# Kernel tuning notes

Measured on AMD Instinct MI355X. Metric: run time of the kernel, lower is better.

## Reference

```python
import jax, jax.numpy as jnp
import numpy as np

B = 2_097_152          # batch of theta samples
POLY_DEG = 127         # QSP polynomial degree -> 128 phases
PI = np.float32(np.pi)


def setup_inputs() -> dict:
    key = jax.random.key(0)
    k1, k2 = jax.random.split(key)
    th = jax.random.uniform(k1, (B, 1), dtype=jnp.float32) * PI
    phis = jax.random.uniform(k2, (POLY_DEG + 1, 1), dtype=jnp.float32) * PI
    return {"th": th, "phis": phis}


def reference(th, phis):
    # th: [B,1] float32, phis: [P+1,1] float32 (learned QSP phases)
    theta = th[:, 0]                      # [B]
    c = jnp.cos(theta)
    s = jnp.sin(theta)
    # expm(i*theta*X) = cos(theta) I + i sin(theta) X  (closed form, no expm)
    wx = jnp.stack(
        [jnp.stack([c + 0j, 1j * s], axis=-1),
         jnp.stack([1j * s, c + 0j], axis=-1)],
        axis=-2,
    ).astype(jnp.complex64)               # [B,2,2]

    phi = phis[:, 0]                      # [P+1]
    e = jnp.exp(1j * phi).astype(jnp.complex64)
    # expm(i*phi*Z) = diag(e^{i phi}, e^{-i phi})
    rz = (jnp.zeros((phi.shape[0], 2, 2), jnp.complex64)
          .at[:, 0, 0].set(e)
          .at[:, 1, 1].set(jnp.conj(e)))  # [P+1,2,2]

    u0 = jnp.broadcast_to(rz[0], (theta.shape[0], 2, 2))  # [B,2,2]

    def step(u, rzk):
        u = jnp.einsum('bij,bjk->bik', u, wx)   # u @ W(x)
        u = jnp.einsum('bij,jk->bik', u, rzk)   # ... @ Rz(phi_k)
        return u, None

    u, _ = jax.lax.scan(step, u0, rz[1:])       # 127 sequential steps
    # convention == 0: (Re[u_00], Im[u_00])
    return (jnp.real(u[:, 0, 0]), jnp.imag(u[:, 0, 0]))
```

## Files before the change

kernel.cpp:

```cpp
#include <hip/hip_runtime.h>


typedef float v2f __attribute__((ext_vector_type(2)));

#define NPHI 128

__global__ __launch_bounds__(256, 8) void qsp_fused(
    const float* __restrict__ th,
    const float* __restrict__ phis,
    float* __restrict__ out,
    int Bq)
{
    __shared__ float2 g2[NPHI];
    __shared__ float2 e[NPHI];

    const int tid = threadIdx.x;

    if (tid < 64) {
        const int L = tid;
        float sp, cp;
        __sincosf(phis[L], &sp, &cp);
        e[L] = make_float2(cp, sp);
        __sincosf(phis[L + 64], &sp, &cp);
        e[L + 64] = make_float2(cp, sp);

        float Ar0 = 0.f, Ai0 = 0.f, Br0 = 0.f, Bi0 = 0.f;
        float Ar1 = 0.f, Ai1 = 0.f, Br1 = 0.f, Bi1 = 0.f;
        const float2 e0 = e[0];
        if (L == 0) { Ar0 = e0.x; Ai0 = e0.y; }

        for (int k = 1; k < NPHI; ++k) {
            const float2 ek = e[k];
            float pAr = __shfl_up(Ar1, 1, 64);
            float pAi = __shfl_up(Ai1, 1, 64);
            float pBr = __shfl_up(Br1, 1, 64);
            float pBi = __shfl_up(Bi1, 1, 64);
            if (L == 0) { pAr = 0.f; pAi = 0.f; pBr = 0.f; pBi = 0.f; }
            const float s0Ar = 0.5f * (pAr + Ar0 + pBr - Br0);
            const float s0Ai = 0.5f * (pAi + Ai0 + pBi - Bi0);
            const float s0Br = 0.5f * (pAr - Ar0 + pBr + Br0);
            const float s0Bi = 0.5f * (pAi - Ai0 + pBi + Bi0);
            const float s1Ar = 0.5f * (Ar0 + Ar1 + Br0 - Br1);
            const float s1Ai = 0.5f * (Ai0 + Ai1 + Bi0 - Bi1);
            const float s1Br = 0.5f * (Ar0 - Ar1 + Br0 + Br1);
            const float s1Bi = 0.5f * (Ai0 - Ai1 + Bi0 + Bi1);
            Ar0 = ek.x * s0Ar - ek.y * s0Ai;  Ai0 = ek.x * s0Ai + ek.y * s0Ar;
            Br0 = ek.x * s0Br + ek.y * s0Bi;  Bi0 = ek.x * s0Bi - ek.y * s0Br;
            Ar1 = ek.x * s1Ar - ek.y * s1Ai;  Ai1 = ek.x * s1Ai + ek.y * s1Ar;
            Br1 = ek.x * s1Br + ek.y * s1Bi;  Bi1 = ek.x * s1Bi - ek.y * s1Br;
        }
        g2[2 * L]     = make_float2(Ar0, Ai0);
        g2[2 * L + 1] = make_float2(Ar1, Ai1);
    }

    const int idx = blockIdx.x * blockDim.x + tid;
    const int lidx = (idx < Bq) ? idx : 0;
    const float4 t4 = ((const float4*)th)[lidx];

    float zs0, zc0, zs1, zc1, zs2, zc2, zs3, zc3;
    __sincosf(2.f * t4.x, &zs0, &zc0);
    __sincosf(2.f * t4.y, &zs1, &zc1);
    __sincosf(2.f * t4.z, &zs2, &zc2);
    __sincosf(2.f * t4.w, &zs3, &zc3);
    const v2f zrA = {zc0, zc1}, ziA = {zs0, zs1}, nziA = {-zs0, -zs1};
    const v2f zrB = {zc2, zc3}, ziB = {zs2, zs3}, nziB = {-zs2, -zs3};

    float S0, C0, S1, C1, S2, C2, S3, C3;
    __sincosf(127.f * t4.x, &S0, &C0);
    __sincosf(127.f * t4.y, &S1, &C1);
    __sincosf(127.f * t4.z, &S2, &C2);
    __sincosf(127.f * t4.w, &S3, &C3);

    __syncthreads();

    const float2 gt = g2[NPHI - 1];
    v2f arA = {gt.x, gt.x}, aiA = {gt.y, gt.y};
    v2f arB = arA,          aiB = aiA;

    #pragma unroll 4
    for (int j = NPHI - 2; j >= 0; --j) {
        const float2 gj = g2[j];
        const v2f gr = {gj.x, gj.x};
        const v2f gi = {gj.y, gj.y};
        const v2f nrA = __builtin_elementwise_fma(
            arA, zrA, __builtin_elementwise_fma(aiA, nziA, gr));
        const v2f niA = __builtin_elementwise_fma(
            arA, ziA, __builtin_elementwise_fma(aiA, zrA, gi));
        const v2f nrB = __builtin_elementwise_fma(
            arB, zrB, __builtin_elementwise_fma(aiB, nziB, gr));
        const v2f niB = __builtin_elementwise_fma(
            arB, ziB, __builtin_elementwise_fma(aiB, zrB, gi));
        arA = nrA; aiA = niA;
        arB = nrB; aiB = niB;
    }

    const v2f CA = {C0, C1}, SA = {S0, S1};
    const v2f CB = {C2, C3}, SB = {S2, S3};
    const v2f orA = __builtin_elementwise_fma(arA, CA, aiA * SA);
    const v2f oiA = __builtin_elementwise_fma(aiA, CA, -(arA * SA));
    const v2f orB = __builtin_elementwise_fma(arB, CB, aiB * SB);
    const v2f oiB = __builtin_elementwise_fma(aiB, CB, -(arB * SB));

    if (idx < Bq) {
        ((float4*)out)[idx]      = make_float4(orA.x, orA.y, orB.x, orB.y);
        ((float4*)out)[idx + Bq] = make_float4(oiA.x, oiA.y, oiB.x, oiB.y);
    }
}

extern "C" void kernel_launch(void* const* d_in, const int* in_sizes, int n_in,
                              void* d_out, int out_size, void* d_ws, size_t ws_size,
                              hipStream_t stream)
{
    const float* th   = (const float*)d_in[0];
    const float* phis = (const float*)d_in[1];
    float* out = (float*)d_out;
    const int B = in_sizes[0];
    const int Bq = B >> 2;
    const int block = 256;
    const int grid = (Bq + block - 1) / block;
    qsp_fused<<<grid, block, 0, stream>>>(th, phis, out, Bq);
}
```

Before: 103.2 us.

## Use 1024-thread blocks and pack-vectorize the per-block phase-coefficient recurrence

Block size grows from 256 to 1024, so the redundant per-block 127-step wavefront that turns phases into polynomial coefficients runs once for every 1024 samples instead of every 256. That recurrence is also rewritten on packed two-float vectors, with the 0.5 factor folded into the precomputed phase exponentials, to cut its instruction count. The costs are a 1024-wide __syncthreads where 960 threads wait on one wavefront, and launch bounds of (1024, 8) that may constrain registers.

```diff
diff --git a/kernel.cpp b/kernel.cpp
--- a/kernel.cpp
+++ b/kernel.cpp
@@ -5,14 +5,14 @@
 
 #define NPHI 128
 
-__global__ __launch_bounds__(256, 8) void qsp_fused(
+__global__ __launch_bounds__(1024, 8) void qsp_fused(
     const float* __restrict__ th,
     const float* __restrict__ phis,
     float* __restrict__ out,
     int Bq)
 {
     __shared__ float2 g2[NPHI];
-    __shared__ float2 e[NPHI];
+    __shared__ float2 h[NPHI];
 
     const int tid = threadIdx.x;
 
@@ -20,37 +20,43 @@
         const int L = tid;
         float sp, cp;
         __sincosf(phis[L], &sp, &cp);
-        e[L] = make_float2(cp, sp);
+        h[L] = make_float2(0.5f * cp, 0.5f * sp);
         __sincosf(phis[L + 64], &sp, &cp);
-        e[L + 64] = make_float2(cp, sp);
+        h[L + 64] = make_float2(0.5f * cp, 0.5f * sp);
 
-        float Ar0 = 0.f, Ai0 = 0.f, Br0 = 0.f, Bi0 = 0.f;
-        float Ar1 = 0.f, Ai1 = 0.f, Br1 = 0.f, Bi1 = 0.f;
-        const float2 e0 = e[0];
-        if (L == 0) { Ar0 = e0.x; Ai0 = e0.y; }
+        v2f A0 = {0.f, 0.f}, B0 = {0.f, 0.f};
+        v2f A1 = {0.f, 0.f}, B1 = {0.f, 0.f};
+        const float2 h0 = h[0];
+        if (L == 0) A0 = (v2f){2.f * h0.x, 2.f * h0.y};
 
+        #pragma unroll 4
         for (int k = 1; k < NPHI; ++k) {
-            const float2 ek = e[k];
-            float pAr = __shfl_up(Ar1, 1, 64);
-            float pAi = __shfl_up(Ai1, 1, 64);
-            float pBr = __shfl_up(Br1, 1, 64);
-            float pBi = __shfl_up(Bi1, 1, 64);
-            if (L == 0) { pAr = 0.f; pAi = 0.f; pBr = 0.f; pBi = 0.f; }
-            const float s0Ar = 0.5f * (pAr + Ar0 + pBr - Br0);
-            const float s0Ai = 0.5f * (pAi + Ai0 + pBi - Bi0);
-            const float s0Br = 0.5f * (pAr - Ar0 + pBr + Br0);
-            const float s0Bi = 0.5f * (pAi - Ai0 + pBi + Bi0);
-            const float s1Ar = 0.5f * (Ar0 + Ar1 + Br0 - Br1);
-            const float s1Ai = 0.5f * (Ai0 + Ai1 + Bi0 - Bi1);
-            const float s1Br = 0.5f * (Ar0 - Ar1 + Br0 + Br1);
-            const float s1Bi = 0.5f * (Ai0 - Ai1 + Bi0 + Bi1);
-            Ar0 = ek.x * s0Ar - ek.y * s0Ai;  Ai0 = ek.x * s0Ai + ek.y * s0Ar;
-            Br0 = ek.x * s0Br + ek.y * s0Bi;  Bi0 = ek.x * s0Bi - ek.y * s0Br;
-            Ar1 = ek.x * s1Ar - ek.y * s1Ai;  Ai1 = ek.x * s1Ai + ek.y * s1Ar;
-            Br1 = ek.x * s1Br + ek.y * s1Bi;  Bi1 = ek.x * s1Bi - ek.y * s1Br;
+            const float2 hk = h[k];
+            const v2f hx  = {hk.x, hk.x};
+            const v2f hyn = {-hk.y, hk.y};
+            const v2f hyp = {hk.y, -hk.y};
+            const float pAr = __shfl_up(A1.x, 1, 64);
+            const float pAi = __shfl_up(A1.y, 1, 64);
+            const float pBr = __shfl_up(B1.x, 1, 64);
+            const float pBi = __shfl_up(B1.y, 1, 64);
+            v2f pA = {pAr, pAi}, pB = {pBr, pBi};
+            if (L == 0) { pA = (v2f){0.f, 0.f}; pB = (v2f){0.f, 0.f}; }
+            const v2f u0 = pA + pB, v0 = A0 - B0;
+            const v2f sA0 = u0 + v0, sB0 = u0 - v0;
+            const v2f u1 = A0 + B0, v1 = A1 - B1;
+            const v2f sA1 = u1 + v1, sB1 = u1 - v1;
+            v2f ts;
+            ts = (v2f){sA0.y, sA0.x};
+            A0 = __builtin_elementwise_fma(hyn, ts, hx * sA0);
+            ts = (v2f){sB0.y, sB0.x};
+            B0 = __builtin_elementwise_fma(hyp, ts, hx * sB0);
+            ts = (v2f){sA1.y, sA1.x};
+            A1 = __builtin_elementwise_fma(hyn, ts, hx * sA1);
+            ts = (v2f){sB1.y, sB1.x};
+            B1 = __builtin_elementwise_fma(hyp, ts, hx * sB1);
         }
-        g2[2 * L]     = make_float2(Ar0, Ai0);
-        g2[2 * L + 1] = make_float2(Ar1, Ai1);
+        g2[2 * L]     = make_float2(A0.x, A0.y);
+        g2[2 * L + 1] = make_float2(A1.x, A1.y);
     }
 
     const int idx = blockIdx.x * blockDim.x + tid;
@@ -116,7 +122,7 @@
     float* out = (float*)d_out;
     const int B = in_sizes[0];
     const int Bq = B >> 2;
-    const int block = 256;
+    const int block = 1024;
     const int grid = (Bq + block - 1) / block;
     qsp_fused<<<grid, block, 0, stream>>>(th, phis, out, Bq);
 }
```

After: 89.91 us. -12.9%, faster.
